# Kernel optimization log

Measured on AMD Instinct MI355X. Metric: run time of the kernel, lower is better.

The kernel has to match this reference:

```python
import jax, jax.numpy as jnp
import numpy as np

# Static model config (matches init_kwargs)
B, N, C = 512, 128, 256          # batch, frames, channels
H, WS = 8, 16                    # num_heads, window_size
HD = C // H                      # head dim
SCALE = HD ** -0.5
NW = N // WS                     # windows per sequence
SHIFTS = (0, WS // 2)            # depth=2: regular block then shifted block
DEPTH = len(SHIFTS)
MLP_HID = 4 * C

# relative_position_index[i, j] = (ws-1) + i - j  (from flipped meshgrid + column distance)
REL_IDX = jnp.asarray((WS - 1) + np.arange(WS)[:, None] - np.arange(WS)[None, :])

# Swin shift attention mask for the shifted block (only last window mixes segments)
def _make_shift_mask(shift):
    img = np.zeros(N)
    img[N - WS:N - shift] = 1
    img[N - shift:] = 2
    mw = img.reshape(NW, WS)
    diff = mw[:, None, :] - mw[:, :, None]   # [w, i, j] = mw[w, j] - mw[w, i]
    return jnp.asarray(np.where(diff != 0, -100.0, 0.0).astype(np.float32))

SHIFT_MASK = _make_shift_mask(SHIFTS[1])     # (NW, WS, WS)


def _ln(x, g, b, eps=1e-5):
    m = jnp.mean(x, axis=-1, keepdims=True)
    v = jnp.mean(jnp.square(x - m), axis=-1, keepdims=True)
    return (x - m) * jax.lax.rsqrt(v + eps) * g + b


def _block(x, g1, b1, qw, qb, pw, pb, rb, g2, b2, f1w, f1b, f2w, f2b, shift):
    h = _ln(x, g1, b1)
    if shift > 0:
        h = jnp.roll(h, -shift, axis=1)
    w = h.reshape(B * NW, WS, C)                              # window partition
    qkv = (w @ qw.T + qb).reshape(B * NW, WS, 3, H, HD)
    q = jnp.moveaxis(qkv[:, :, 0], 1, 2)                      # (BnW, H, WS, HD)
    k = jnp.moveaxis(qkv[:, :, 1], 1, 2)
    v = jnp.moveaxis(qkv[:, :, 2], 1, 2)
    attn = jnp.einsum('bhid,bhjd->bhij', q * SCALE, k)        # (BnW, H, WS, WS)
    bias = jnp.transpose(rb[REL_IDX], (2, 0, 1))              # (H, WS, WS)
    attn = attn + bias[None]
    if shift > 0:
        attn = attn.reshape(B, NW, H, WS, WS) + SHIFT_MASK[None, :, None]
        attn = attn.reshape(B * NW, H, WS, WS)
    attn = jax.nn.softmax(attn, axis=-1)
    o = jnp.einsum('bhij,bhjd->bhid', attn, v)
    o = jnp.moveaxis(o, 1, 2).reshape(B * NW, WS, C)
    o = o @ pw.T + pb
    o = o.reshape(B, N, C)                                    # window reverse
    if shift > 0:
        o = jnp.roll(o, shift, axis=1)
    x = x + o                                                 # residual (drop_path=0)
    h = _ln(x, g2, b2)
    h = jax.nn.gelu(h @ f1w.T + f1b, approximate=False)       # torch GELU is exact erf
    return x + h @ f2w.T + f2b


def setup_inputs() -> dict:
    key = jax.random.key(0)
    ks = jax.random.split(key, 8)
    s = 0.02
    return {
        'x': jax.random.normal(ks[0], (B, N, C), jnp.float32),
        'ln1_g': jnp.ones((DEPTH, C), jnp.float32),
        'ln1_b': jnp.zeros((DEPTH, C), jnp.float32),
        'qkv_w': jax.random.normal(ks[1], (DEPTH, 3 * C, C), jnp.float32) * s,
        'qkv_b': jnp.zeros((DEPTH, 3 * C), jnp.float32),
        'proj_w': jax.random.normal(ks[2], (DEPTH, C, C), jnp.float32) * s,
        'proj_b': jnp.zeros((DEPTH, C), jnp.float32),
        'rel_bias': jax.random.normal(ks[3], (DEPTH, 2 * WS - 1, H), jnp.float32) * s,
        'ln2_g': jnp.ones((DEPTH, C), jnp.float32),
        'ln2_b': jnp.zeros((DEPTH, C), jnp.float32),
        'fc1_w': jax.random.normal(ks[4], (DEPTH, MLP_HID, C), jnp.float32) * s,
        'fc1_b': jnp.zeros((DEPTH, MLP_HID), jnp.float32),
        'fc2_w': jax.random.normal(ks[5], (DEPTH, C, MLP_HID), jnp.float32) * s,
        'fc2_b': jnp.zeros((DEPTH, C), jnp.float32),
    }


def reference(x, ln1_g, ln1_b, qkv_w, qkv_b, proj_w, proj_b, rel_bias,
              ln2_g, ln2_b, fc1_w, fc1_b, fc2_w, fc2_b):
    for i, shift in enumerate(SHIFTS):
        x = _block(x, ln1_g[i], ln1_b[i], qkv_w[i], qkv_b[i], proj_w[i], proj_b[i],
                   rel_bias[i], ln2_g[i], ln2_b[i], fc1_w[i], fc1_b[i],
                   fc2_w[i], fc2_b[i], shift)
    return x
```

## Files before the change

kernel.cpp:

```cpp
#include <hip/hip_runtime.h>
#include <cstdint>
#include <cstddef>

#define B_    512
#define N_    128
#define C_    256
#define H_    8
#define WSZ   16
#define HD    32
#define NW    8
#define M_TOT 65536

typedef __bf16 bf16x8 __attribute__((ext_vector_type(8)));
typedef float  f32x4  __attribute__((ext_vector_type(4)));
typedef unsigned short u16;
typedef unsigned int   u32;

__device__ __forceinline__ float bf2f(u16 v){
  union { u32 u; float f; } c; c.u = ((u32)v) << 16; return c.f;
}
__device__ __forceinline__ u16 f2bf(float f){
  union { float f; u32 u; } c; c.f = f;
  return (u16)((c.u + 0x7FFFu + ((c.u >> 16) & 1u)) >> 16);
}

__device__ __forceinline__ void gload_lds16(const void* g, void* l){
  __builtin_amdgcn_global_load_lds(
      (const __attribute__((address_space(1))) u32*)g,
      (__attribute__((address_space(3))) u32*)l, 16, 0, 0);
}

__device__ __forceinline__ void unpack8(uint4 r, float* d){
  d[0]=bf2f((u16)(r.x & 0xFFFFu)); d[1]=bf2f((u16)(r.x >> 16));
  d[2]=bf2f((u16)(r.y & 0xFFFFu)); d[3]=bf2f((u16)(r.y >> 16));
  d[4]=bf2f((u16)(r.z & 0xFFFFu)); d[5]=bf2f((u16)(r.z >> 16));
  d[6]=bf2f((u16)(r.w & 0xFFFFu)); d[7]=bf2f((u16)(r.w >> 16));
}

__global__ __launch_bounds__(256) void ln_kernel(const float* __restrict__ x,
    const float* __restrict__ g, const float* __restrict__ b,
    u16* __restrict__ out, int shift)
{
  int lane = threadIdx.x & 63;
  int row  = blockIdx.x * 4 + (threadIdx.x >> 6);
  int in_row = (row & ~(N_-1)) | ((row + shift) & (N_-1));
  float4 xv = *reinterpret_cast<const float4*>(x + (size_t)in_row * C_ + lane * 4);
  float s  = xv.x + xv.y + xv.z + xv.w;
  float s2 = xv.x*xv.x + xv.y*xv.y + xv.z*xv.z + xv.w*xv.w;
  #pragma unroll
  for (int off = 1; off < 64; off <<= 1){ s += __shfl_xor(s, off); s2 += __shfl_xor(s2, off); }
  float mean = s * (1.f / C_);
  float inv  = rsqrtf(s2 * (1.f / C_) - mean * mean + 1e-5f);
  float4 gv = *reinterpret_cast<const float4*>(g + lane * 4);
  float4 bv = *reinterpret_cast<const float4*>(b + lane * 4);
  ushort4 o;
  o.x = f2bf((xv.x - mean) * inv * gv.x + bv.x);
  o.y = f2bf((xv.y - mean) * inv * gv.y + bv.y);
  o.z = f2bf((xv.z - mean) * inv * gv.z + bv.z);
  o.w = f2bf((xv.w - mean) * inv * gv.w + bv.w);
  *reinterpret_cast<ushort4*>(out + (size_t)row * C_ + lane * 4) = o;
}

__global__ __launch_bounds__(256) void cvt_kernel(const float* __restrict__ s,
                                                  u16* __restrict__ d, int n4)
{
  int i = blockIdx.x * 256 + threadIdx.x;
  if (i >= n4) return;
  float4 v = reinterpret_cast<const float4*>(s)[i];
  ushort4 o; o.x=f2bf(v.x); o.y=f2bf(v.y); o.z=f2bf(v.z); o.w=f2bf(v.w);
  reinterpret_cast<ushort4*>(d)[i] = o;
}

template<int EPI, int K, int NN>
__global__ __launch_bounds__(256) void gemm_kernel(const u16* __restrict__ A,
    const u16* __restrict__ W, const float* __restrict__ bias,
    u16* __restrict__ outb, float* __restrict__ outf, const float* __restrict__ resid,
    int Nout, int shift)
{
  __shared__ __align__(16) u16 Al[128 * 64];
  __shared__ __align__(16) u16 Bl[128 * 64];
  int lane = threadIdx.x & 63, wv = threadIdx.x >> 6;
  int wm = (wv >> 1) * 64, wn = (wv & 1) * 64;

  int nwg = gridDim.x;
  int nid = (blockIdx.x & 7) * (nwg >> 3) + (blockIdx.x >> 3);
  int bm = nid / NN, bn = nid % NN;

  size_t Abase = (size_t)bm * 128 * K;
  size_t Wbase = (size_t)bn * 128 * K;

  f32x4 acc[4][4];
  #pragma unroll
  for (int mi = 0; mi < 4; mi++)
    #pragma unroll
    for (int ni = 0; ni < 4; ni++)
      #pragma unroll
      for (int r = 0; r < 4; r++) acc[mi][ni][r] = 0.f;

  int r0 = wv * 32;
  int srow = lane >> 3;
  int scol = ((lane & 7) ^ (lane >> 3)) * 8;

  for (int kt = 0; kt < K; kt += 64){
    __syncthreads();
    #pragma unroll
    for (int t = 0; t < 4; t++){
      int row = r0 + t * 8 + srow;
      gload_lds16(A + Abase + (size_t)row * K + kt + scol, &Al[(r0 + t * 8) * 64]);
      gload_lds16(W + Wbase + (size_t)row * K + kt + scol, &Bl[(r0 + t * 8) * 64]);
    }
    __syncthreads();
    #pragma unroll
    for (int kk = 0; kk < 64; kk += 32){
      int j = (kk >> 3) + (lane >> 4);
      int ko = ((j ^ (lane & 7)) << 3);
      bf16x8 af[4], bfr[4];
      #pragma unroll
      for (int mi = 0; mi < 4; mi++)
        af[mi] = *reinterpret_cast<const bf16x8*>(&Al[(wm + mi * 16 + (lane & 15)) * 64 + ko]);
      #pragma unroll
      for (int ni = 0; ni < 4; ni++)
        bfr[ni] = *reinterpret_cast<const bf16x8*>(&Bl[(wn + ni * 16 + (lane & 15)) * 64 + ko]);
      #pragma unroll
      for (int mi = 0; mi < 4; mi++)
        #pragma unroll
        for (int ni = 0; ni < 4; ni++)
          acc[mi][ni] = __builtin_amdgcn_mfma_f32_16x16x32_bf16(af[mi], bfr[ni], acc[mi][ni], 0, 0, 0);
    }
  }
  int col0 = bn * 128 + wn + (lane & 15);
  float bv[4];
  #pragma unroll
  for (int ni = 0; ni < 4; ni++) bv[ni] = bias[col0 + ni * 16];
  int rbase = bm * 128 + wm + (lane >> 4) * 4;
  #pragma unroll
  for (int mi = 0; mi < 4; mi++){
    #pragma unroll
    for (int r = 0; r < 4; r++){
      int m = rbase + mi * 16 + r;
      #pragma unroll
      for (int ni = 0; ni < 4; ni++){
        float v = acc[mi][ni][r] + bv[ni];
        int n = col0 + ni * 16;
        if (EPI == 0){
          outb[(size_t)m * Nout + n] = f2bf(v);
        } else if (EPI == 1){
          v = 0.5f * v * (1.f + erff(v * 0.70710678118654752f));
          outb[(size_t)m * Nout + n] = f2bf(v);
        } else if (EPI == 2){
          size_t idx = (size_t)((m & ~(N_-1)) | ((m + shift) & (N_-1))) * Nout + n;
          outf[idx] = v + resid[idx];
        } else {
          size_t idx = (size_t)m * Nout + n;
          outf[idx] = v + resid[idx];
        }
      }
    }
  }
}

__global__ __launch_bounds__(512) void attn_kernel(const u16* __restrict__ qkv,
    const float* __restrict__ rb, u16* __restrict__ o, int shifted)
{
  __shared__ float q_s[H_][WSZ][36];
  __shared__ float k_s[H_][WSZ][36];
  __shared__ float v_s[H_][WSZ][36];
  __shared__ float p_s[H_][WSZ][17];
  int h = threadIdx.x >> 6, lane = threadIdx.x & 63;
  int i = lane >> 2, c8 = (lane & 3) * 8;
  int m0 = blockIdx.x * WSZ;
  size_t base = (size_t)(m0 + i) * 768 + h * HD + c8;
  uint4 rq = *reinterpret_cast<const uint4*>(qkv + base);
  uint4 rk = *reinterpret_cast<const uint4*>(qkv + base + 256);
  uint4 rv = *reinterpret_cast<const uint4*>(qkv + base + 512);
  unpack8(rq, &q_s[h][i][c8]);
  unpack8(rk, &k_s[h][i][c8]);
  unpack8(rv, &v_s[h][i][c8]);
  __syncthreads();

  float qv[HD];
  #pragma unroll
  for (int d4 = 0; d4 < 8; d4++){
    float4 t = *reinterpret_cast<const float4*>(&q_s[h][i][d4 * 4]);
    qv[d4*4+0] = t.x; qv[d4*4+1] = t.y; qv[d4*4+2] = t.z; qv[d4*4+3] = t.w;
  }

  int j0 = (lane & 3) * 4;
  bool lastw = shifted && ((blockIdx.x & (NW - 1)) == NW - 1);
  float p[4];
  #pragma unroll
  for (int jj = 0; jj < 4; jj++){
    int j = j0 + jj;
    float d = 0.f;
    #pragma unroll
    for (int d4 = 0; d4 < 8; d4++){
      float4 kv = *reinterpret_cast<const float4*>(&k_s[h][j][d4 * 4]);
      d += qv[d4*4+0]*kv.x + qv[d4*4+1]*kv.y + qv[d4*4+2]*kv.z + qv[d4*4+3]*kv.w;
    }
    d *= 0.17677669529663689f;
    d += rb[(15 + i - j) * H_ + h];
    if (lastw && ((i < 8) != (j < 8))) d -= 100.f;
    p[jj] = d;
  }
  float mx = fmaxf(fmaxf(p[0], p[1]), fmaxf(p[2], p[3]));
  mx = fmaxf(mx, __shfl_xor(mx, 1));
  mx = fmaxf(mx, __shfl_xor(mx, 2));
  float sum = 0.f;
  #pragma unroll
  for (int jj = 0; jj < 4; jj++){ p[jj] = expf(p[jj] - mx); sum += p[jj]; }
  sum += __shfl_xor(sum, 1);
  sum += __shfl_xor(sum, 2);
  float inv = 1.f / sum;
  #pragma unroll
  for (int jj = 0; jj < 4; jj++) p_s[h][i][j0 + jj] = p[jj] * inv;
  __syncthreads();

  float4 a0 = {0.f,0.f,0.f,0.f}, a1 = {0.f,0.f,0.f,0.f};
  #pragma unroll
  for (int j = 0; j < WSZ; j++){
    float pv = p_s[h][i][j];
    float4 v0 = *reinterpret_cast<const float4*>(&v_s[h][j][c8]);
    float4 v1 = *reinterpret_cast<const float4*>(&v_s[h][j][c8 + 4]);
    a0.x += pv*v0.x; a0.y += pv*v0.y; a0.z += pv*v0.z; a0.w += pv*v0.w;
    a1.x += pv*v1.x; a1.y += pv*v1.y; a1.z += pv*v1.z; a1.w += pv*v1.w;
  }
  uint4 w;
  w.x = (u32)f2bf(a0.x) | ((u32)f2bf(a0.y) << 16);
  w.y = (u32)f2bf(a0.z) | ((u32)f2bf(a0.w) << 16);
  w.z = (u32)f2bf(a1.x) | ((u32)f2bf(a1.y) << 16);
  w.w = (u32)f2bf(a1.z) | ((u32)f2bf(a1.w) << 16);
  *reinterpret_cast<uint4*>(o + (size_t)(m0 + i) * C_ + h * HD + c8) = w;
}

extern "C" void kernel_launch(void* const* d_in, const int* in_sizes, int n_in,
                              void* d_out, int out_size, void* d_ws, size_t ws_size,
                              hipStream_t stream)
{
  const float* x      = (const float*)d_in[0];
  const float* ln1_g  = (const float*)d_in[1];
  const float* ln1_b  = (const float*)d_in[2];
  const float* qkv_w  = (const float*)d_in[3];
  const float* qkv_b  = (const float*)d_in[4];
  const float* proj_w = (const float*)d_in[5];
  const float* proj_b = (const float*)d_in[6];
  const float* rel_b  = (const float*)d_in[7];
  const float* ln2_g  = (const float*)d_in[8];
  const float* ln2_b  = (const float*)d_in[9];
  const float* fc1_w  = (const float*)d_in[10];
  const float* fc1_b  = (const float*)d_in[11];
  const float* fc2_w  = (const float*)d_in[12];
  const float* fc2_b  = (const float*)d_in[13];
  float* out = (float*)d_out;
  char*  ws  = (char*)d_ws;

  u16* qkv_wb  = (u16*)ws;
  u16* proj_wb = qkv_wb + 393216;
  u16* fc1_wb  = proj_wb + 131072;
  u16* fc2_wb  = fc1_wb + 524288;
  u16* h_buf   = (u16*)(ws + (  4ull << 20));
  u16* qkv_buf = (u16*)(ws + ( 36ull << 20));
  u16* o_buf   = (u16*)(ws + (132ull << 20));
  u16* h2_buf  = h_buf;
  u16* u_buf   = qkv_buf;

  cvt_kernel<<<384, 256, 0, stream>>>(qkv_w,  qkv_wb,  393216 / 4);
  cvt_kernel<<<128, 256, 0, stream>>>(proj_w, proj_wb, 131072 / 4);
  cvt_kernel<<<512, 256, 0, stream>>>(fc1_w,  fc1_wb,  524288 / 4);
  cvt_kernel<<<512, 256, 0, stream>>>(fc2_w,  fc2_wb,  524288 / 4);

  const float* xin = x;
  for (int d = 0; d < 2; d++){
    int shift = d ? (WSZ / 2) : 0;
    ln_kernel<<<M_TOT / 4, 256, 0, stream>>>(xin, ln1_g + d * C_, ln1_b + d * C_,
        h_buf, shift);
    gemm_kernel<0, 256, 6><<<512 * 6, 256, 0, stream>>>(h_buf, qkv_wb + d * 196608,
        qkv_b + d * 768, qkv_buf, nullptr, nullptr, 768, 0);
    attn_kernel<<<M_TOT / WSZ, 512, 0, stream>>>(qkv_buf, rel_b + d * 248, o_buf,
        shift ? 1 : 0);
    gemm_kernel<2, 256, 2><<<512 * 2, 256, 0, stream>>>(o_buf, proj_wb + d * 65536,
        proj_b + d * C_, nullptr, out, xin, C_, shift);
    ln_kernel<<<M_TOT / 4, 256, 0, stream>>>(out, ln2_g + d * C_, ln2_b + d * C_,
        h2_buf, 0);
    gemm_kernel<1, 256, 8><<<512 * 8, 256, 0, stream>>>(h2_buf, fc1_wb + d * 262144,
        fc1_b + d * 1024, u_buf, nullptr, nullptr, 1024, 0);
    gemm_kernel<3, 1024, 2><<<512 * 2, 256, 0, stream>>>(u_buf, fc2_wb + d * 262144,
        fc2_b + d * C_, nullptr, out, out, C_, 0);
    xin = out;
  }
}
```

Measured before the change: 693.9 us.

## Fuse MLP fc1+GELU+fc2 into one kernel keeping hidden activations in LDS

```diff
diff --git a/kernel.cpp b/kernel.cpp
--- a/kernel.cpp
+++ b/kernel.cpp
@@ -36,6 +36,10 @@
   d[4]=bf2f((u16)(r.z & 0xFFFFu)); d[5]=bf2f((u16)(r.z >> 16));
   d[6]=bf2f((u16)(r.w & 0xFFFFu)); d[7]=bf2f((u16)(r.w >> 16));
 }
+
+__device__ __forceinline__ void vmcnt4(){ asm volatile("s_waitcnt vmcnt(4)" ::: "memory"); }
+__device__ __forceinline__ void vmcnt0(){ asm volatile("s_waitcnt vmcnt(0)" ::: "memory"); }
+__device__ __forceinline__ void lgkm0(){ asm volatile("s_waitcnt lgkmcnt(0)" ::: "memory"); }
 
 __global__ __launch_bounds__(256) void ln_kernel(const float* __restrict__ x,
     const float* __restrict__ g, const float* __restrict__ b,
@@ -144,16 +148,160 @@
         int n = col0 + ni * 16;
         if (EPI == 0){
           outb[(size_t)m * Nout + n] = f2bf(v);
-        } else if (EPI == 1){
-          v = 0.5f * v * (1.f + erff(v * 0.70710678118654752f));
-          outb[(size_t)m * Nout + n] = f2bf(v);
-        } else if (EPI == 2){
+        } else {
           size_t idx = (size_t)((m & ~(N_-1)) | ((m + shift) & (N_-1))) * Nout + n;
           outf[idx] = v + resid[idx];
-        } else {
-          size_t idx = (size_t)m * Nout + n;
-          outf[idx] = v + resid[idx];
         }
+      }
+    }
+  }
+}
+
+__global__ __launch_bounds__(512, 2) void mlp_kernel(const u16* __restrict__ h2,
+    const u16* __restrict__ W1, const float* __restrict__ b1,
+    const u16* __restrict__ W2, const float* __restrict__ b2,
+    float* __restrict__ out)
+{
+  __shared__ __align__(16) u16 As[128 * 64];
+  __shared__ __align__(16) u16 Ws[2][256 * 64];
+  __shared__ __align__(16) u16 Us[128 * 256];
+
+  int lane = threadIdx.x & 63, wv = threadIdx.x >> 6;
+  int wm = (wv >> 2) * 64;
+  int wn = (wv & 3) * 64;
+  int m0 = blockIdx.x * 128;
+  int srow = lane >> 3;
+  int swz = ((lane & 7) ^ (lane >> 3)) * 8;
+
+  auto stage_A = [&](int kt){
+    #pragma unroll
+    for (int i = 0; i < 2; i++){
+      int rb = wv * 16 + i * 8;
+      gload_lds16(h2 + (size_t)(m0 + rb + srow) * 256 + kt * 64 + swz, &As[rb * 64]);
+    }
+  };
+  auto stage_W = [&](int buf, const u16* Wp, int kstride, int gcol0){
+    #pragma unroll
+    for (int i = 0; i < 4; i++){
+      int rb = wv * 32 + i * 8;
+      gload_lds16(Wp + (size_t)(rb + srow) * kstride + gcol0 + swz, &Ws[buf][rb * 64]);
+    }
+  };
+
+  f32x4 acc2[4][4];
+  #pragma unroll
+  for (int mi = 0; mi < 4; mi++)
+    #pragma unroll
+    for (int ni = 0; ni < 4; ni++)
+      #pragma unroll
+      for (int r = 0; r < 4; r++) acc2[mi][ni][r] = 0.f;
+
+  stage_W(0, W1, 256, 0);
+  #pragma unroll 1
+  for (int p = 0; p < 4; p++){
+    const u16* W1p = W1 + (size_t)p * 65536;
+    f32x4 acc1[4][4];
+    #pragma unroll
+    for (int mi = 0; mi < 4; mi++)
+      #pragma unroll
+      for (int ni = 0; ni < 4; ni++)
+        #pragma unroll
+        for (int r = 0; r < 4; r++) acc1[mi][ni][r] = 0.f;
+
+    #pragma unroll 1
+    for (int kt = 0; kt < 4; kt++){
+      __builtin_amdgcn_s_barrier();
+      stage_A(kt);
+      if (kt < 3) stage_W((kt + 1) & 1, W1p, 256, (kt + 1) * 64);
+      else        stage_W(0, W2, 1024, p * 256);
+      vmcnt4();
+      __builtin_amdgcn_s_barrier();
+      __builtin_amdgcn_sched_barrier(0);
+      int cur = kt & 1;
+      #pragma unroll
+      for (int kk = 0; kk < 64; kk += 32){
+        int j = (kk >> 3) + (lane >> 4);
+        int ko = ((j ^ (lane & 7)) << 3);
+        bf16x8 af[4], bfr[4];
+        #pragma unroll
+        for (int mi = 0; mi < 4; mi++)
+          af[mi] = *reinterpret_cast<const bf16x8*>(&As[(wm + mi * 16 + (lane & 15)) * 64 + ko]);
+        #pragma unroll
+        for (int ni = 0; ni < 4; ni++)
+          bfr[ni] = *reinterpret_cast<const bf16x8*>(&Ws[cur][(wn + ni * 16 + (lane & 15)) * 64 + ko]);
+        #pragma unroll
+        for (int mi = 0; mi < 4; mi++)
+          #pragma unroll
+          for (int ni = 0; ni < 4; ni++)
+            acc1[mi][ni] = __builtin_amdgcn_mfma_f32_16x16x32_bf16(af[mi], bfr[ni], acc1[mi][ni], 0, 0, 0);
+      }
+    }
+
+    {
+      float b1v[4];
+      #pragma unroll
+      for (int ni = 0; ni < 4; ni++) b1v[ni] = b1[p * 256 + wn + ni * 16 + (lane & 15)];
+      #pragma unroll
+      for (int mi = 0; mi < 4; mi++){
+        #pragma unroll
+        for (int ni = 0; ni < 4; ni++){
+          #pragma unroll
+          for (int r = 0; r < 4; r++){
+            int m = wm + mi * 16 + (lane >> 4) * 4 + r;
+            int n = wn + ni * 16 + (lane & 15);
+            float u = acc1[mi][ni][r] + b1v[ni];
+            u = 0.5f * u * (1.f + erff(u * 0.70710678118654752f));
+            Us[m * 256 + (((n >> 3) ^ (m & 7)) << 3) + (n & 7)] = f2bf(u);
+          }
+        }
+      }
+    }
+    lgkm0();
+
+    #pragma unroll 1
+    for (int kt2 = 0; kt2 < 4; kt2++){
+      __builtin_amdgcn_s_barrier();
+      if (kt2 < 3)      stage_W((kt2 + 1) & 1, W2, 1024, p * 256 + (kt2 + 1) * 64);
+      else if (p < 3)   stage_W(0, W1 + (size_t)(p + 1) * 65536, 256, 0);
+      if (p == 3 && kt2 == 3) vmcnt0(); else vmcnt4();
+      __builtin_amdgcn_s_barrier();
+      __builtin_amdgcn_sched_barrier(0);
+      int cur = kt2 & 1;
+      #pragma unroll
+      for (int kk = 0; kk < 64; kk += 32){
+        int j2 = kt2 * 8 + (kk >> 3) + (lane >> 4);
+        int ko = (((kk >> 3) + (lane >> 4)) ^ (lane & 7)) << 3;
+        bf16x8 af[4], bfr[4];
+        #pragma unroll
+        for (int mi = 0; mi < 4; mi++){
+          int m = wm + mi * 16 + (lane & 15);
+          af[mi] = *reinterpret_cast<const bf16x8*>(&Us[m * 256 + ((j2 ^ (lane & 7)) << 3)]);
+        }
+        #pragma unroll
+        for (int ni = 0; ni < 4; ni++)
+          bfr[ni] = *reinterpret_cast<const bf16x8*>(&Ws[cur][(wn + ni * 16 + (lane & 15)) * 64 + ko]);
+        #pragma unroll
+        for (int mi = 0; mi < 4; mi++)
+          #pragma unroll
+          for (int ni = 0; ni < 4; ni++)
+            acc2[mi][ni] = __builtin_amdgcn_mfma_f32_16x16x32_bf16(af[mi], bfr[ni], acc2[mi][ni], 0, 0, 0);
+      }
+    }
+  }
+
+  float b2v[4];
+  #pragma unroll
+  for (int ni = 0; ni < 4; ni++) b2v[ni] = b2[wn + ni * 16 + (lane & 15)];
+  #pragma unroll
+  for (int mi = 0; mi < 4; mi++){
+    #pragma unroll
+    for (int r = 0; r < 4; r++){
+      int m = m0 + wm + mi * 16 + (lane >> 4) * 4 + r;
+      #pragma unroll
+      for (int ni = 0; ni < 4; ni++){
+        int n = wn + ni * 16 + (lane & 15);
+        size_t idx = (size_t)m * 256 + n;
+        out[idx] = out[idx] + acc2[mi][ni][r] + b2v[ni];
       }
     }
   }
@@ -261,7 +409,6 @@
   u16* qkv_buf = (u16*)(ws + ( 36ull << 20));
   u16* o_buf   = (u16*)(ws + (132ull << 20));
   u16* h2_buf  = h_buf;
-  u16* u_buf   = qkv_buf;
 
   cvt_kernel<<<384, 256, 0, stream>>>(qkv_w,  qkv_wb,  393216 / 4);
   cvt_kernel<<<128, 256, 0, stream>>>(proj_w, proj_wb, 131072 / 4);
@@ -281,10 +428,8 @@
         proj_b + d * C_, nullptr, out, xin, C_, shift);
     ln_kernel<<<M_TOT / 4, 256, 0, stream>>>(out, ln2_g + d * C_, ln2_b + d * C_,
         h2_buf, 0);
-    gemm_kernel<1, 256, 8><<<512 * 8, 256, 0, stream>>>(h2_buf, fc1_wb + d * 262144,
-        fc1_b + d * 1024, u_buf, nullptr, nullptr, 1024, 0);
-    gemm_kernel<3, 1024, 2><<<512 * 2, 256, 0, stream>>>(u_buf, fc2_wb + d * 262144,
-        fc2_b + d * C_, nullptr, out, out, C_, 0);
+    mlp_kernel<<<M_TOT / 128, 512, 0, stream>>>(h2_buf, fc1_wb + d * 262144,
+        fc1_b + d * 1024, fc2_wb + d * 262144, fc2_b + d * C_, out);
     xin = out;
   }
 }
```

After: 732.6 us. 1.06x slower.
